# Performance work log

Hardware: AMD Instinct MI355X
Metric: run time of the kernel (lower is better)

## Reference

```python
import jax, jax.numpy as jnp
import numpy as np

N, C = 8, 3
HD, WD = 1024, 1280   # camera (depth) resolution
HS, WS = 800, 1280    # projector pattern resolution


def _build_calib():
    fx, fy, dx, dy = 1200.0, 1200.0, 640.0, 512.0
    ww = np.arange(WD, dtype=np.float32)[None, :].repeat(HD, 0)
    hh = np.arange(HD, dtype=np.float32)[:, None].repeat(WD, 1)
    vec = np.stack([(ww - dx) / fx, (hh - dy) / fy, np.ones_like(ww)], axis=2)  # [H,W,3]
    th = 0.15
    ext_rot = np.array([[np.cos(th), 0.0, np.sin(th)],
                        [0.0, 1.0, 0.0],
                        [-np.sin(th), 0.0, np.cos(th)]], np.float32)
    abc = np.einsum('ij,hwj->hwi', ext_rot, vec).astype(np.float32)  # [H,W,3]
    abc_mat = np.transpose(abc, (2, 0, 1))  # [3,H,W] (plb.a2t HWC->CHW)
    ext_tran = np.array([200.0, 0.0, 50.0], np.float32)
    pat_intrin = np.array([1100.0, 1100.0, 640.0, 400.0], np.float32)
    return abc_mat, ext_tran, pat_intrin


def setup_inputs() -> dict:
    key = jax.random.key(0)
    k1, k2 = jax.random.split(key)
    abc, tr, pi = _build_calib()
    depth_mat = 500.0 + 500.0 * jax.random.uniform(k1, (N, 1, HD, WD), jnp.float32)
    src_mat = jax.random.normal(k2, (N, C, HS, WS), jnp.float32)
    return {"depth_mat": depth_mat, "src_mat": src_mat,
            "abc_mat": jnp.asarray(abc), "ext_tran": jnp.asarray(tr),
            "pat_intrin": jnp.asarray(pi)}


def _grid_sample_border(src, gx, gy):
    # src: [N,C,Hs,Ws]; gx,gy: [N,H,W] normalized grid; bilinear,
    # align_corners=False, padding_mode='border' (torch semantics).
    n, c, hs, ws = src.shape
    x = ((gx + 1.0) * ws - 1.0) * 0.5
    y = ((gy + 1.0) * hs - 1.0) * 0.5
    x = jnp.clip(x, 0.0, ws - 1.0)
    y = jnp.clip(y, 0.0, hs - 1.0)
    x0 = jnp.floor(x)
    y0 = jnp.floor(y)
    wx = x - x0
    wy = y - y0
    x0i = x0.astype(jnp.int32)
    y0i = y0.astype(jnp.int32)
    x1i = jnp.minimum(x0i + 1, ws - 1)
    y1i = jnp.minimum(y0i + 1, hs - 1)
    b = jnp.arange(n)[:, None, None]

    def g(yi, xi):
        return src[b, :, yi, xi]  # [N,H,W,C]

    out = (g(y0i, x0i) * ((1.0 - wy) * (1.0 - wx))[..., None]
           + g(y0i, x1i) * ((1.0 - wy) * wx)[..., None]
           + g(y1i, x0i) * (wy * (1.0 - wx))[..., None]
           + g(y1i, x1i) * (wy * wx)[..., None])
    return jnp.transpose(out, (0, 3, 1, 2))  # [N,C,H,W]


def reference(depth_mat, src_mat, abc_mat, ext_tran, pat_intrin):
    hs, ws = src_mat.shape[-2:]
    denom = abc_mat[2] * depth_mat + ext_tran[2]          # [N,1,H,W]
    xx = (abc_mat[0] * depth_mat + ext_tran[0]) / denom
    yy = (abc_mat[1] * depth_mat + ext_tran[1]) / denom
    fu, fv, du, dv = pat_intrin
    uu = fu * xx + du
    vv = fv * yy + dv
    # NOTE: original normalizes by (size-1) even with align_corners=False;
    # replicated faithfully.
    gx = 2.0 * uu[:, 0] / (ws - 1) - 1.0                  # [N,H,W]
    gy = 2.0 * vv[:, 0] / (hs - 1) - 1.0
    return _grid_sample_border(src_mat, gx, gy)
```

## Files before the change

kernel.cpp:

```cpp
#include <hip/hip_runtime.h>

#define N_  8
#define C_  3
#define HD_ 1024
#define WD_ 1280
#define HS_ 800
#define WS_ 1280

typedef float fx4 __attribute__((ext_vector_type(4)));
typedef unsigned int u32x4 __attribute__((ext_vector_type(4)));
typedef u32x4 u32x4a8 __attribute__((aligned(8)));

__device__ __forceinline__ unsigned short f2bf(float f) {
    unsigned int u = __float_as_uint(f);
    unsigned int r = (u + 0x7FFFu + ((u >> 16) & 1u)) >> 16;
    return (unsigned short)r;
}
__device__ __forceinline__ float bf2f(unsigned int h) {
    return __uint_as_float(h << 16);
}

__device__ __forceinline__ int xcd_chunk_swizzle(int bid, int nwg) {
    const int NX = 8;
    int q = nwg / NX, r = nwg % NX;
    int xcd = bid % NX;
    int lid = bid / NX;
    return (xcd < r) ? (xcd * (q + 1) + lid)
                     : (r * (q + 1) + (xcd - r) * q + lid);
}

__global__ __launch_bounds__(256) void interleave_kernel(
    const float* __restrict__ src, uint4* __restrict__ ws)
{
    const size_t HWs = (size_t)HS_ * WS_;
    size_t g = (size_t)blockIdx.x * blockDim.x + threadIdx.x;
    size_t base = g * 4;
    if (base >= (size_t)N_ * HWs) return;
    int n = (int)(base / HWs);
    size_t p = base - (size_t)n * HWs;
    const float* s = src + (size_t)n * C_ * HWs + p;
    fx4 c0 = __builtin_nontemporal_load((const fx4*)(s));
    fx4 c1 = __builtin_nontemporal_load((const fx4*)(s + HWs));
    fx4 c2 = __builtin_nontemporal_load((const fx4*)(s + 2 * HWs));

    uint4 A, B;
    A.x = (unsigned)f2bf(c0.x) | ((unsigned)f2bf(c1.x) << 16);
    A.y = (unsigned)f2bf(c2.x);
    A.z = (unsigned)f2bf(c0.y) | ((unsigned)f2bf(c1.y) << 16);
    A.w = (unsigned)f2bf(c2.y);
    B.x = (unsigned)f2bf(c0.z) | ((unsigned)f2bf(c1.z) << 16);
    B.y = (unsigned)f2bf(c2.z);
    B.z = (unsigned)f2bf(c0.w) | ((unsigned)f2bf(c1.w) << 16);
    B.w = (unsigned)f2bf(c2.w);

    size_t o = base / 2;
    ws[o]     = A;
    ws[o + 1] = B;
}

__global__ __launch_bounds__(256) void warp_main_kernel(
    const float* __restrict__ depth,
    const uint2* __restrict__ wsrc,
    const float* __restrict__ abc,
    const float* __restrict__ tr,
    const float* __restrict__ pin,
    float* __restrict__ out)
{
    const int HW = HD_ * WD_;
    int swz = xcd_chunk_swizzle(blockIdx.x, gridDim.x);
    int idx = swz * blockDim.x + threadIdx.x;
    if (idx >= N_ * HW) return;

    int n  = idx / HW;
    int hw = idx - n * HW;

    float d = __builtin_nontemporal_load(&depth[idx]);
    float a = abc[hw];
    float b = abc[HW + hw];
    float c = abc[2 * HW + hw];

    float tx = tr[0], ty = tr[1], tz = tr[2];
    float fu = pin[0], fv = pin[1], du = pin[2], dv = pin[3];

    float denom = c * d + tz;
    float inv = 1.0f / denom;
    float xx = (a * d + tx) * inv;
    float yy = (b * d + ty) * inv;
    float uu = fu * xx + du;
    float vv = fv * yy + dv;

    float gx = 2.0f * uu / (float)(WS_ - 1) - 1.0f;
    float gy = 2.0f * vv / (float)(HS_ - 1) - 1.0f;
    float x = ((gx + 1.0f) * (float)WS_ - 1.0f) * 0.5f;
    float y = ((gy + 1.0f) * (float)HS_ - 1.0f) * 0.5f;

    x = fminf(fmaxf(x, 0.0f), (float)(WS_ - 1));
    y = fminf(fmaxf(y, 0.0f), (float)(HS_ - 1));

    int x0 = min((int)floorf(x), WS_ - 2);
    int y0 = min((int)floorf(y), HS_ - 2);
    float wx = x - (float)x0;
    float wy = y - (float)y0;

    float w00 = (1.0f - wy) * (1.0f - wx);
    float w01 = (1.0f - wy) * wx;
    float w10 = wy * (1.0f - wx);
    float w11 = wy * wx;

    const size_t HWs = (size_t)HS_ * WS_;
    const uint2* sn = wsrc + (size_t)n * HWs;
    u32x4 r0 = *(const u32x4a8*)(sn + (size_t)y0 * WS_ + x0);
    u32x4 r1 = *(const u32x4a8*)(sn + (size_t)(y0 + 1) * WS_ + x0);

    float* on = out + (size_t)n * C_ * HW + hw;

    float v0 = bf2f(r0.x & 0xFFFFu) * w00 + bf2f(r0.z & 0xFFFFu) * w01
             + bf2f(r1.x & 0xFFFFu) * w10 + bf2f(r1.z & 0xFFFFu) * w11;
    float v1 = bf2f(r0.x >> 16) * w00 + bf2f(r0.z >> 16) * w01
             + bf2f(r1.x >> 16) * w10 + bf2f(r1.z >> 16) * w11;
    float v2 = bf2f(r0.y & 0xFFFFu) * w00 + bf2f(r0.w & 0xFFFFu) * w01
             + bf2f(r1.y & 0xFFFFu) * w10 + bf2f(r1.w & 0xFFFFu) * w11;

    __builtin_nontemporal_store(v0, on);
    __builtin_nontemporal_store(v1, on + (size_t)HW);
    __builtin_nontemporal_store(v2, on + (size_t)2 * HW);
}

__global__ __launch_bounds__(256) void warp_planar_kernel(
    const float* __restrict__ depth, const float* __restrict__ src,
    const float* __restrict__ abc, const float* __restrict__ tr,
    const float* __restrict__ pin, float* __restrict__ out)
{
    const int HW = HD_ * WD_;
    int idx = blockIdx.x * blockDim.x + threadIdx.x;
    if (idx >= N_ * HW) return;
    int n  = idx / HW;
    int hw = idx - n * HW;
    float d = depth[idx];
    float a = abc[hw];
    float b = abc[HW + hw];
    float c = abc[2 * HW + hw];
    float denom = c * d + tr[2];
    float inv = 1.0f / denom;
    float uu = pin[0] * ((a * d + tr[0]) * inv) + pin[2];
    float vv = pin[1] * ((b * d + tr[1]) * inv) + pin[3];
    float gx = 2.0f * uu / (float)(WS_ - 1) - 1.0f;
    float gy = 2.0f * vv / (float)(HS_ - 1) - 1.0f;
    float x = ((gx + 1.0f) * (float)WS_ - 1.0f) * 0.5f;
    float y = ((gy + 1.0f) * (float)HS_ - 1.0f) * 0.5f;
    x = fminf(fmaxf(x, 0.0f), (float)(WS_ - 1));
    y = fminf(fmaxf(y, 0.0f), (float)(HS_ - 1));
    float x0f = floorf(x), y0f = floorf(y);
    float wx = x - x0f, wy = y - y0f;
    int x0 = (int)x0f, y0 = (int)y0f;
    int x1 = min(x0 + 1, WS_ - 1);
    int y1 = min(y0 + 1, HS_ - 1);
    float w00 = (1.0f - wy) * (1.0f - wx), w01 = (1.0f - wy) * wx;
    float w10 = wy * (1.0f - wx), w11 = wy * wx;
    const size_t HWs = (size_t)HS_ * WS_;
    const float* sn = src + (size_t)n * C_ * HWs;
    int o00 = y0 * WS_ + x0, o01 = y0 * WS_ + x1;
    int o10 = y1 * WS_ + x0, o11 = y1 * WS_ + x1;
    float* on = out + (size_t)n * C_ * HW + hw;
#pragma unroll
    for (int ch = 0; ch < C_; ++ch) {
        const float* sc = sn + (size_t)ch * HWs;
        on[(size_t)ch * HW] = sc[o00] * w00 + sc[o01] * w01
                            + sc[o10] * w10 + sc[o11] * w11;
    }
}

extern "C" void kernel_launch(void* const* d_in, const int* in_sizes, int n_in,
                              void* d_out, int out_size, void* d_ws, size_t ws_size,
                              hipStream_t stream) {
    const float* depth = (const float*)d_in[0];
    const float* src   = (const float*)d_in[1];
    const float* abc   = (const float*)d_in[2];
    const float* tr    = (const float*)d_in[3];
    const float* pin   = (const float*)d_in[4];
    float* out = (float*)d_out;

    const size_t need = (size_t)N_ * HS_ * WS_ * 8;
    const int total = N_ * HD_ * WD_;
    const int block = 256;

    if (ws_size >= need) {
        const size_t src_px = (size_t)N_ * HS_ * WS_;
        const int g1 = (int)((src_px / 4 + block - 1) / block);
        interleave_kernel<<<g1, block, 0, stream>>>(src, (uint4*)d_ws);
        const int g2 = (total + block - 1) / block;
        warp_main_kernel<<<g2, block, 0, stream>>>(depth, (const uint2*)d_ws,
                                                   abc, tr, pin, out);
    } else {
        const int g = (total + block - 1) / block;
        warp_planar_kernel<<<g, block, 0, stream>>>(depth, src, abc, tr, pin, out);
    }
}
```

Baseline: 296.3 us.

## Pack both bilinear source rows into one 16-byte texel for single-row gathers

Adds a pre-pass that stores, for each source pixel, the bf16 values of all three channels for that row and the row below, making each workspace texel 16 bytes. The warp kernel then fetches two adjacent 16-byte texels instead of two row-separated 16-byte reads, so each lookup touches one contiguous 32-byte span and spatial locality in the gather improves. The cost is twice the workspace traffic in the pre-pass (write 16 bytes per pixel and read six float4s), and the path is taken only when the workspace is large enough.

```diff
diff --git a/kernel.cpp b/kernel.cpp
--- a/kernel.cpp
+++ b/kernel.cpp
@@ -27,6 +27,121 @@
     int lid = bid / NX;
     return (xcd < r) ? (xcd * (q + 1) + lid)
                      : (r * (q + 1) + (xcd - r) * q + lid);
+}
+
+__global__ __launch_bounds__(256) void interleave2_kernel(
+    const float* __restrict__ src, uint4* __restrict__ ws)
+{
+    const size_t HWs = (size_t)HS_ * WS_;
+    int swz = xcd_chunk_swizzle(blockIdx.x, gridDim.x);
+    size_t g = (size_t)swz * blockDim.x + threadIdx.x;
+    size_t base = g * 4;
+    if (base >= (size_t)N_ * HWs) return;
+    int n = (int)(base / HWs);
+    size_t p = base - (size_t)n * HWs;
+    int r = (int)(p / WS_);
+    size_t xoff = p - (size_t)r * WS_;
+    int r1 = min(r + 1, HS_ - 1);
+
+    const float* sn = src + (size_t)n * C_ * HWs;
+    const float* s0 = sn + p;
+    const float* s1 = sn + (size_t)r1 * WS_ + xoff;
+    fx4 a0 = *(const fx4*)(s0);
+    fx4 a1 = *(const fx4*)(s0 + HWs);
+    fx4 a2 = *(const fx4*)(s0 + 2 * HWs);
+    fx4 b0 = *(const fx4*)(s1);
+    fx4 b1 = *(const fx4*)(s1 + HWs);
+    fx4 b2 = *(const fx4*)(s1 + 2 * HWs);
+
+    uint4 u0, u1, u2, u3;
+    u0.x = (unsigned)f2bf(a0.x) | ((unsigned)f2bf(a1.x) << 16);
+    u0.y = (unsigned)f2bf(a2.x);
+    u0.z = (unsigned)f2bf(b0.x) | ((unsigned)f2bf(b1.x) << 16);
+    u0.w = (unsigned)f2bf(b2.x);
+    u1.x = (unsigned)f2bf(a0.y) | ((unsigned)f2bf(a1.y) << 16);
+    u1.y = (unsigned)f2bf(a2.y);
+    u1.z = (unsigned)f2bf(b0.y) | ((unsigned)f2bf(b1.y) << 16);
+    u1.w = (unsigned)f2bf(b2.y);
+    u2.x = (unsigned)f2bf(a0.z) | ((unsigned)f2bf(a1.z) << 16);
+    u2.y = (unsigned)f2bf(a2.z);
+    u2.z = (unsigned)f2bf(b0.z) | ((unsigned)f2bf(b1.z) << 16);
+    u2.w = (unsigned)f2bf(b2.z);
+    u3.x = (unsigned)f2bf(a0.w) | ((unsigned)f2bf(a1.w) << 16);
+    u3.y = (unsigned)f2bf(a2.w);
+    u3.z = (unsigned)f2bf(b0.w) | ((unsigned)f2bf(b1.w) << 16);
+    u3.w = (unsigned)f2bf(b2.w);
+
+    uint4* W = ws + base;
+    W[0] = u0; W[1] = u1; W[2] = u2; W[3] = u3;
+}
+
+__global__ __launch_bounds__(256) void warp_main2_kernel(
+    const float* __restrict__ depth,
+    const uint4* __restrict__ wsrc,
+    const float* __restrict__ abc,
+    const float* __restrict__ tr,
+    const float* __restrict__ pin,
+    float* __restrict__ out)
+{
+    const int HW = HD_ * WD_;
+    int swz = xcd_chunk_swizzle(blockIdx.x, gridDim.x);
+    int idx = swz * blockDim.x + threadIdx.x;
+    if (idx >= N_ * HW) return;
+
+    int n  = idx / HW;
+    int hw = idx - n * HW;
+
+    float d = __builtin_nontemporal_load(&depth[idx]);
+    float a = abc[hw];
+    float b = abc[HW + hw];
+    float c = abc[2 * HW + hw];
+
+    float tx = tr[0], ty = tr[1], tz = tr[2];
+    float fu = pin[0], fv = pin[1], du = pin[2], dv = pin[3];
+
+    float denom = c * d + tz;
+    float inv = 1.0f / denom;
+    float xx = (a * d + tx) * inv;
+    float yy = (b * d + ty) * inv;
+    float uu = fu * xx + du;
+    float vv = fv * yy + dv;
+
+    float gx = 2.0f * uu / (float)(WS_ - 1) - 1.0f;
+    float gy = 2.0f * vv / (float)(HS_ - 1) - 1.0f;
+    float x = ((gx + 1.0f) * (float)WS_ - 1.0f) * 0.5f;
+    float y = ((gy + 1.0f) * (float)HS_ - 1.0f) * 0.5f;
+
+    x = fminf(fmaxf(x, 0.0f), (float)(WS_ - 1));
+    y = fminf(fmaxf(y, 0.0f), (float)(HS_ - 1));
+
+    int x0 = min((int)floorf(x), WS_ - 2);
+    int y0 = min((int)floorf(y), HS_ - 2);
+    float wx = x - (float)x0;
+    float wy = y - (float)y0;
+
+    float w00 = (1.0f - wy) * (1.0f - wx);
+    float w01 = (1.0f - wy) * wx;
+    float w10 = wy * (1.0f - wx);
+    float w11 = wy * wx;
+
+    const size_t HWs = (size_t)HS_ * WS_;
+    const uint4* sn = wsrc + (size_t)n * HWs;
+    size_t u = (size_t)y0 * WS_ + x0;
+    uint4 q0 = sn[u];
+    uint4 q1 = sn[u + 1];
+
+    float* on = out + (size_t)n * C_ * HW + hw;
+
+    float v0 = bf2f(q0.x & 0xFFFFu) * w00 + bf2f(q1.x & 0xFFFFu) * w01
+             + bf2f(q0.z & 0xFFFFu) * w10 + bf2f(q1.z & 0xFFFFu) * w11;
+    float v1 = bf2f(q0.x >> 16) * w00 + bf2f(q1.x >> 16) * w01
+             + bf2f(q0.z >> 16) * w10 + bf2f(q1.z >> 16) * w11;
+    float v2 = bf2f(q0.y & 0xFFFFu) * w00 + bf2f(q1.y & 0xFFFFu) * w01
+             + bf2f(q0.w & 0xFFFFu) * w10 + bf2f(q1.w & 0xFFFFu) * w11;
+
+    __builtin_nontemporal_store(v0, on);
+    __builtin_nontemporal_store(v1, on + (size_t)HW);
+    __builtin_nontemporal_store(v2, on + (size_t)2 * HW);
 }
 
 __global__ __launch_bounds__(256) void interleave_kernel(
@@ -59,68 +174,53 @@
 }
 
 __global__ __launch_bounds__(256) void warp_main_kernel(
-    const float* __restrict__ depth,
-    const uint2* __restrict__ wsrc,
-    const float* __restrict__ abc,
-    const float* __restrict__ tr,
-    const float* __restrict__ pin,
-    float* __restrict__ out)
+    const float* __restrict__ depth, const uint2* __restrict__ wsrc,
+    const float* __restrict__ abc, const float* __restrict__ tr,
+    const float* __restrict__ pin, float* __restrict__ out)
 {
     const int HW = HD_ * WD_;
     int swz = xcd_chunk_swizzle(blockIdx.x, gridDim.x);
     int idx = swz * blockDim.x + threadIdx.x;
     if (idx >= N_ * HW) return;
-
     int n  = idx / HW;
     int hw = idx - n * HW;
-
     float d = __builtin_nontemporal_load(&depth[idx]);
     float a = abc[hw];
     float b = abc[HW + hw];
     float c = abc[2 * HW + hw];
-
     float tx = tr[0], ty = tr[1], tz = tr[2];
     float fu = pin[0], fv = pin[1], du = pin[2], dv = pin[3];
-
     float denom = c * d + tz;
     float inv = 1.0f / denom;
     float xx = (a * d + tx) * inv;
     float yy = (b * d + ty) * inv;
     float uu = fu * xx + du;
     float vv = fv * yy + dv;
-
     float gx = 2.0f * uu / (float)(WS_ - 1) - 1.0f;
     float gy = 2.0f * vv / (float)(HS_ - 1) - 1.0f;
     float x = ((gx + 1.0f) * (float)WS_ - 1.0f) * 0.5f;
     float y = ((gy + 1.0f) * (float)HS_ - 1.0f) * 0.5f;
-
     x = fminf(fmaxf(x, 0.0f), (float)(WS_ - 1));
     y = fminf(fmaxf(y, 0.0f), (float)(HS_ - 1));
-
     int x0 = min((int)floorf(x), WS_ - 2);
     int y0 = min((int)floorf(y), HS_ - 2);
     float wx = x - (float)x0;
     float wy = y - (float)y0;
-
     float w00 = (1.0f - wy) * (1.0f - wx);
     float w01 = (1.0f - wy) * wx;
     float w10 = wy * (1.0f - wx);
     float w11 = wy * wx;
-
     const size_t HWs = (size_t)HS_ * WS_;
     const uint2* sn = wsrc + (size_t)n * HWs;
     u32x4 r0 = *(const u32x4a8*)(sn + (size_t)y0 * WS_ + x0);
     u32x4 r1 = *(const u32x4a8*)(sn + (size_t)(y0 + 1) * WS_ + x0);
-
     float* on = out + (size_t)n * C_ * HW + hw;
-
     float v0 = bf2f(r0.x & 0xFFFFu) * w00 + bf2f(r0.z & 0xFFFFu) * w01
              + bf2f(r1.x & 0xFFFFu) * w10 + bf2f(r1.z & 0xFFFFu) * w11;
     float v1 = bf2f(r0.x >> 16) * w00 + bf2f(r0.z >> 16) * w01
              + bf2f(r1.x >> 16) * w10 + bf2f(r1.z >> 16) * w11;
     float v2 = bf2f(r0.y & 0xFFFFu) * w00 + bf2f(r0.w & 0xFFFFu) * w01
              + bf2f(r1.y & 0xFFFFu) * w10 + bf2f(r1.w & 0xFFFFu) * w11;
-
     __builtin_nontemporal_store(v0, on);
     __builtin_nontemporal_store(v1, on + (size_t)HW);
     __builtin_nontemporal_store(v2, on + (size_t)2 * HW);
@@ -180,19 +280,24 @@
     const float* pin   = (const float*)d_in[4];
     float* out = (float*)d_out;
 
-    const size_t need = (size_t)N_ * HS_ * WS_ * 8;
+    const size_t src_px = (size_t)N_ * HS_ * WS_;
+    const size_t need16 = src_px * 16;
+    const size_t need8  = src_px * 8;
     const int total = N_ * HD_ * WD_;
     const int block = 256;
-
-    if (ws_size >= need) {
-        const size_t src_px = (size_t)N_ * HS_ * WS_;
+    const int g2 = (total + block - 1) / block;
+
+    if (ws_size >= need16) {
+        const int g1 = (int)((src_px / 4 + block - 1) / block);
+        interleave2_kernel<<<g1, block, 0, stream>>>(src, (uint4*)d_ws);
+        warp_main2_kernel<<<g2, block, 0, stream>>>(depth, (const uint4*)d_ws,
+                                                    abc, tr, pin, out);
+    } else if (ws_size >= need8) {
         const int g1 = (int)((src_px / 4 + block - 1) / block);
         interleave_kernel<<<g1, block, 0, stream>>>(src, (uint4*)d_ws);
-        const int g2 = (total + block - 1) / block;
         warp_main_kernel<<<g2, block, 0, stream>>>(depth, (const uint2*)d_ws,
                                                    abc, tr, pin, out);
     } else {
-        const int g = (total + block - 1) / block;
-        warp_planar_kernel<<<g, block, 0, stream>>>(depth, src, abc, tr, pin, out);
+        warp_planar_kernel<<<g2, block, 0, stream>>>(depth, src, abc, tr, pin, out);
     }
 }
```

Result: slower. 320.4 us (+8.2%).
